# Optimization experiments

Measured on AMD Instinct MI355X. Metric: run time of the kernel, lower is better.

## Reference

```python
import jax, jax.numpy as jnp
import numpy as np

N_NODES = 100000
N_EDGES = 1600000
IN_CH, HID_CH, OUT_CH = 128, 128, 64
N_GRAPHS = 64


def gcn_conv(x, src, dst, W, b, n_nodes):
    """PyG-style GCNConv: self-loops already included in (src, dst).
    out_i = b + sum_j norm_ij * (x_j @ W), norm_ij = deg_i^-1/2 * deg_j^-1/2."""
    xw = x @ W  # [N, out]
    deg = jax.ops.segment_sum(jnp.ones_like(dst, dtype=xw.dtype), dst,
                              num_segments=n_nodes)  # [N]
    dinv = jnp.where(deg > 0, jax.lax.rsqrt(jnp.maximum(deg, 1e-12)), 0.0)
    norm = dinv[src] * dinv[dst]  # [E]
    msg = xw[src] * norm[:, None]  # gather + scale  [E, out]
    out = jax.ops.segment_sum(msg, dst, num_segments=n_nodes)  # scatter-add
    return out + b


def global_mean_pool(x, batch, n_graphs):
    s = jax.ops.segment_sum(x, batch, num_segments=n_graphs)
    cnt = jax.ops.segment_sum(jnp.ones((x.shape[0],), x.dtype), batch,
                              num_segments=n_graphs)
    return s / jnp.maximum(cnt, 1.0)[:, None]


def setup_inputs() -> dict:
    key = jax.random.key(0)
    ks = jax.random.split(key, 9)
    x = jax.random.normal(ks[0], (N_NODES, IN_CH), dtype=jnp.float32)
    edge_index = jax.random.randint(ks[1], (2, N_EDGES), 0, N_NODES, dtype=jnp.int64)
    batch = jnp.sort(jax.random.randint(ks[2], (N_NODES,), 0, N_GRAPHS, dtype=jnp.int64))
    # Glorot-ish params
    s1 = 1.0 / np.sqrt(IN_CH)
    s2 = 1.0 / np.sqrt(HID_CH)
    W1 = jax.random.normal(ks[3], (IN_CH, HID_CH), jnp.float32) * s1
    b1 = jnp.zeros((HID_CH,), jnp.float32)
    W2 = jax.random.normal(ks[4], (HID_CH, HID_CH), jnp.float32) * s2
    b2 = jnp.zeros((HID_CH,), jnp.float32)
    Wl = jax.random.normal(ks[5], (HID_CH, OUT_CH), jnp.float32) * s2
    bl = jax.random.normal(ks[6], (OUT_CH,), jnp.float32) * 0.01
    return {"x": x, "edge_index": edge_index, "batch": batch,
            "W1": W1, "b1": b1, "W2": W2, "b2": b2, "Wl": Wl, "bl": bl}


def reference(x, edge_index, batch, W1, b1, W2, b2, Wl, bl):
    n = x.shape[0]
    loop = jnp.arange(n, dtype=edge_index.dtype)
    src = jnp.concatenate([edge_index[0], loop])  # add self-loops
    dst = jnp.concatenate([edge_index[1], loop])
    h = jax.nn.relu(gcn_conv(x, src, dst, W1, b1, n))
    h = jax.nn.relu(gcn_conv(h, src, dst, W2, b2, n))
    g = global_mean_pool(h, batch, N_GRAPHS)  # [B, hid]
    return g @ Wl + bl  # [B, out]
```

## Files before the change

### kernel.cpp

```cpp
#include <hip/hip_runtime.h>

#define N_NODESC 100000
#define N_EDGESC 1600000
#define CH 128
#define NG 64
#define OC 64

#define GST_BLKS 391
#define EDGE_BLKS 6250
#define MFMA_BLKS 1563
#define PAD_STRIDE 128
#define RANGE 12500
#define EB_PER_BLK 16
#define BGROUPS ((EDGE_BLKS + EB_PER_BLK - 1) / EB_PER_BLK)
#define BUILD_BLKS (8 * BGROUPS)

typedef __attribute__((ext_vector_type(8))) short short8;
typedef __attribute__((ext_vector_type(4))) float f32x4;

__device__ __forceinline__ unsigned short f2b_u(float f) {
    union { float f; unsigned int u; } x; x.f = f;
    unsigned int u = x.u;
    return (unsigned short)((u + 0x7fffu + ((u >> 16) & 1u)) >> 16);
}
__device__ __forceinline__ float b2f_lo(unsigned int v) {
    union { unsigned int u; float f; } x; x.u = v << 16; return x.f;
}
__device__ __forceinline__ float b2f_hi(unsigned int v) {
    union { unsigned int u; float f; } x; x.u = v & 0xffff0000u; return x.f;
}
__device__ __forceinline__ float dinv_of(const int* __restrict__ deg, int i) {
    return rsqrtf((float)(deg[i] + 1));
}

#define WSTR 136
template<int AFP>
__device__ __forceinline__ void mfma_compute(int blk, int t, const void* __restrict__ Ap,
                                             unsigned short* __restrict__ Ob,
                                             const unsigned short* WsT) {
    int wave = t >> 6, lane = t & 63;
    int quad = lane >> 4, l16 = lane & 15;
    int arow = blk * 64 + wave * 16 + l16;
    bool rowok = arow < N_NODESC;
    f32x4 acc[8] = {};
#pragma unroll
    for (int c = 0; c < 4; ++c) {
        int koff = c * 32 + quad * 8;
        short8 a;
        if (AFP) {
            const float* A = (const float*)Ap;
            float4 f0 = make_float4(0, 0, 0, 0), f1 = make_float4(0, 0, 0, 0);
            if (rowok) {
                f0 = *(const float4*)(A + (size_t)arow * 128 + koff);
                f1 = *(const float4*)(A + (size_t)arow * 128 + koff + 4);
            }
            a[0] = (short)f2b_u(f0.x); a[1] = (short)f2b_u(f0.y);
            a[2] = (short)f2b_u(f0.z); a[3] = (short)f2b_u(f0.w);
            a[4] = (short)f2b_u(f1.x); a[5] = (short)f2b_u(f1.y);
            a[6] = (short)f2b_u(f1.z); a[7] = (short)f2b_u(f1.w);
        } else {
            const unsigned short* A = (const unsigned short*)Ap;
            if (rowok) a = *(const short8*)(A + (size_t)arow * 128 + koff);
            else       a = (short8)(short)0;
        }
#pragma unroll
        for (int tt = 0; tt < 8; ++tt) {
            short8 b = *(const short8*)&WsT[(tt * 16 + l16) * WSTR + koff];
            acc[tt] = __builtin_amdgcn_mfma_f32_16x16x32_bf16(a, b, acc[tt], 0, 0, 0);
        }
    }
    int orow0 = blk * 64 + wave * 16 + quad * 4;
#pragma unroll
    for (int r = 0; r < 4; ++r) {
        int g = orow0 + r;
        if (g < N_NODESC) {
#pragma unroll
            for (int tt = 0; tt < 8; ++tt)
                Ob[(size_t)g * 128 + tt * 16 + l16] = f2b_u(acc[tt][r]);
        }
    }
}

__global__ void k_pack(const float* __restrict__ W2, const int* __restrict__ batch,
                       unsigned short* __restrict__ Wt2, int* __restrict__ gstart) {
    int b = blockIdx.x, t = threadIdx.x;
    if (b < 64) {
        int i = b * 256 + t;
        int k = i >> 7, c = i & 127;
        Wt2[c * 128 + k] = f2b_u(W2[k * 128 + c]);
    } else {
        int i = (b - 64) * 256 + t;
        if (i >= N_NODESC) return;
        int bb = batch[i];
        int bp = (i == 0) ? -1 : batch[i - 1];
        for (int g = bp + 1; g <= bb; ++g) gstart[g] = i;
        if (i == N_NODESC - 1)
            for (int g = bb + 1; g <= NG; ++g) gstart[g] = N_NODESC;
    }
}

__global__ __launch_bounds__(256) void k_l1_build(const float* __restrict__ x,
                                                  const float* __restrict__ W1,
                                                  unsigned short* __restrict__ xw,
                                                  const int* __restrict__ ei,
                                                  int* __restrict__ deg,
                                                  int* __restrict__ pad) {
    __shared__ unsigned short WsT[128 * WSTR];
    int t = threadIdx.x;
    if (blockIdx.x < BUILD_BLKS) {
        int bb = blockIdx.x;
        unsigned int r = bb & 7;
        int g0 = (bb >> 3) * EB_PER_BLK;
#pragma unroll 4
        for (int i = 0; i < EB_PER_BLK; ++i) {
            int e = (g0 + i) * 256 + t;
            if (e < N_EDGESC) {
                int d = ei[N_EDGESC + e];
                if ((unsigned)d / RANGE == r) {
                    int slot = atomicAdd(&deg[d], 1);
                    pad[d * PAD_STRIDE + (slot & (PAD_STRIDE - 1))] = ei[e];
                }
            }
        }
    } else {
        int blk = blockIdx.x - BUILD_BLKS;
        for (int idx = t; idx < 16384; idx += 256) {
            int k = idx >> 7, c = idx & 127;
            WsT[c * WSTR + k] = f2b_u(W1[idx]);
        }
        __syncthreads();
        mfma_compute<1>(blk, t, x, xw, WsT);
    }
}

__global__ __launch_bounds__(256) void k_mfma2(const unsigned short* __restrict__ A,
                                               const unsigned short* __restrict__ Wt,
                                               unsigned short* __restrict__ Ob) {
    __shared__ unsigned short WsT[128 * WSTR];
    int t = threadIdx.x;
    {
        const uint4* wsrc = (const uint4*)Wt;
        for (int idx = t; idx < 2048; idx += 256) {
            int row = idx >> 4, sub = idx & 15;
            *((uint4*)&WsT[row * WSTR] + sub) = wsrc[row * 16 + sub];
        }
    }
    __syncthreads();
    mfma_compute<0>(blockIdx.x, t, A, Ob, WsT);
}

__device__ __forceinline__ void gather_row(const unsigned int* __restrict__ xw,
                                           const int* __restrict__ pad,
                                           const int* __restrict__ deg,
                                           int s, int e, int lane,
                                           float& acc0, float& acc1) {
    int i = s;
    for (; i + 8 <= e; i += 8) {
        int s0 = pad[i], s1 = pad[i + 1], s2 = pad[i + 2], s3 = pad[i + 3];
        int s4 = pad[i + 4], s5 = pad[i + 5], s6 = pad[i + 6], s7 = pad[i + 7];
        float w0 = dinv_of(deg, s0), w1 = dinv_of(deg, s1);
        float w2 = dinv_of(deg, s2), w3 = dinv_of(deg, s3);
        float w4 = dinv_of(deg, s4), w5 = dinv_of(deg, s5);
        float w6 = dinv_of(deg, s6), w7 = dinv_of(deg, s7);
        unsigned int v0 = xw[(size_t)s0 * 64 + lane];
        unsigned int v1 = xw[(size_t)s1 * 64 + lane];
        unsigned int v2 = xw[(size_t)s2 * 64 + lane];
        unsigned int v3 = xw[(size_t)s3 * 64 + lane];
        unsigned int v4 = xw[(size_t)s4 * 64 + lane];
        unsigned int v5 = xw[(size_t)s5 * 64 + lane];
        unsigned int v6 = xw[(size_t)s6 * 64 + lane];
        unsigned int v7 = xw[(size_t)s7 * 64 + lane];
        acc0 += w0 * b2f_lo(v0); acc1 += w0 * b2f_hi(v0);
        acc0 += w1 * b2f_lo(v1); acc1 += w1 * b2f_hi(v1);
        acc0 += w2 * b2f_lo(v2); acc1 += w2 * b2f_hi(v2);
        acc0 += w3 * b2f_lo(v3); acc1 += w3 * b2f_hi(v3);
        acc0 += w4 * b2f_lo(v4); acc1 += w4 * b2f_hi(v4);
        acc0 += w5 * b2f_lo(v5); acc1 += w5 * b2f_hi(v5);
        acc0 += w6 * b2f_lo(v6); acc1 += w6 * b2f_hi(v6);
        acc0 += w7 * b2f_lo(v7); acc1 += w7 * b2f_hi(v7);
    }
    for (; i + 4 <= e; i += 4) {
        int s0 = pad[i], s1 = pad[i + 1], s2 = pad[i + 2], s3 = pad[i + 3];
        float w0 = dinv_of(deg, s0), w1 = dinv_of(deg, s1);
        float w2 = dinv_of(deg, s2), w3 = dinv_of(deg, s3);
        unsigned int v0 = xw[(size_t)s0 * 64 + lane];
        unsigned int v1 = xw[(size_t)s1 * 64 + lane];
        unsigned int v2 = xw[(size_t)s2 * 64 + lane];
        unsigned int v3 = xw[(size_t)s3 * 64 + lane];
        acc0 += w0 * b2f_lo(v0); acc1 += w0 * b2f_hi(v0);
        acc0 += w1 * b2f_lo(v1); acc1 += w1 * b2f_hi(v1);
        acc0 += w2 * b2f_lo(v2); acc1 += w2 * b2f_hi(v2);
        acc0 += w3 * b2f_lo(v3); acc1 += w3 * b2f_hi(v3);
    }
    for (; i < e; ++i) {
        int s0 = pad[i];
        float w0 = dinv_of(deg, s0);
        unsigned int v0 = xw[(size_t)s0 * 64 + lane];
        acc0 += w0 * b2f_lo(v0); acc1 += w0 * b2f_hi(v0);
    }
}

__global__ __launch_bounds__(256) void k_gather1(const unsigned int* __restrict__ xw,
                                                 const int* __restrict__ deg,
                                                 const int* __restrict__ pad,
                                                 const float* __restrict__ bias,
                                                 unsigned int* __restrict__ outp) {
    int t = threadIdx.x;
    int lane = t & 63;
    int node = blockIdx.x * 4 + (t >> 6);
    if (node >= N_NODESC) return;
    int dg = deg[node];
    int s = node * PAD_STRIDE, e = s + dg;
    float wn = rsqrtf((float)(dg + 1));
    unsigned int vs = xw[(size_t)node * 64 + lane];
    float acc0 = wn * b2f_lo(vs), acc1 = wn * b2f_hi(vs);
    gather_row(xw, pad, deg, s, e, lane, acc0, acc1);
    float2 b = ((const float2*)bias)[lane];
    float o0 = fmaxf(b.x + wn * acc0, 0.f);
    float o1 = fmaxf(b.y + wn * acc1, 0.f);
    outp[(size_t)node * 64 + lane] =
        ((unsigned int)f2b_u(o1) << 16) | (unsigned int)f2b_u(o0);
}

__global__ __launch_bounds__(256) void k_gather_pool(const unsigned int* __restrict__ xw,
                                                     const int* __restrict__ deg,
                                                     const int* __restrict__ pad,
                                                     const float* __restrict__ bias,
                                                     const int* __restrict__ batch,
                                                     float* __restrict__ gpart) {
    __shared__ float lds[4 * 128];
    int t = threadIdx.x, w = t >> 6, lane = t & 63;
    int base = blockIdx.x * 16;
    bool fast = batch[base] == batch[base + 15];
    float2 bv = ((const float2*)bias)[lane];
    float sum0 = 0.f, sum1 = 0.f;
#pragma unroll 1
    for (int j = 0; j < 4; ++j) {
        int node = base + w * 4 + j;
        int dg = deg[node];
        int s = node * PAD_STRIDE, e = s + dg;
        float wn = rsqrtf((float)(dg + 1));
        unsigned int vs = xw[(size_t)node * 64 + lane];
        float acc0 = wn * b2f_lo(vs), acc1 = wn * b2f_hi(vs);
        gather_row(xw, pad, deg, s, e, lane, acc0, acc1);
        float o0 = fmaxf(bv.x + wn * acc0, 0.f);
        float o1 = fmaxf(bv.y + wn * acc1, 0.f);
        if (fast) {
            sum0 += o0; sum1 += o1;
        } else {
            int g = batch[node];
            atomicAdd(&gpart[g * 128 + lane * 2], o0);
            atomicAdd(&gpart[g * 128 + lane * 2 + 1], o1);
        }
    }
    if (fast) {
        lds[w * 128 + lane * 2] = sum0;
        lds[w * 128 + lane * 2 + 1] = sum1;
        __syncthreads();
        if (t < 128) {
            float v = lds[t] + lds[128 + t] + lds[256 + t] + lds[384 + t];
            atomicAdd(&gpart[batch[base] * 128 + t], v);
        }
    }
}

__global__ void k_final(const float* __restrict__ gpart, const int* __restrict__ gstart,
                        const float* __restrict__ Wl, const float* __restrict__ bl,
                        float* __restrict__ out) {
    __shared__ float gs[128];
    int b = blockIdx.x;
    int o = threadIdx.x;
    gs[o] = gpart[b * 128 + o];
    gs[o + 64] = gpart[b * 128 + 64 + o];
    __syncthreads();
    int cnt = gstart[b + 1] - gstart[b];
    float sc = 1.f / (float)(cnt > 0 ? cnt : 1);
    float sum = 0.f;
    for (int k = 0; k < 128; ++k) sum += gs[k] * Wl[k * 64 + o];
    out[b * 64 + o] = bl[o] + sc * sum;
}

extern "C" void kernel_launch(void* const* d_in, const int* in_sizes, int n_in,
                              void* d_out, int out_size, void* d_ws, size_t ws_size,
                              hipStream_t stream) {
    const float* x    = (const float*)d_in[0];
    const int*   ei   = (const int*)d_in[1];
    const int*   batch= (const int*)d_in[2];
    const float* W1   = (const float*)d_in[3];
    const float* b1   = (const float*)d_in[4];
    const float* W2   = (const float*)d_in[5];
    const float* b2   = (const float*)d_in[6];
    const float* Wl   = (const float*)d_in[7];
    const float* bl   = (const float*)d_in[8];
    float* out = (float*)d_out;

    char* ws = (char*)d_ws;
    unsigned short* xw_s = (unsigned short*)ws; ws += (size_t)N_NODESC * CH * 2;
    unsigned short* h_b  = (unsigned short*)ws; ws += (size_t)N_NODESC * CH * 2;
    unsigned short* Wt2 = (unsigned short*)ws; ws += (size_t)CH * CH * 2;
    int*   deg    = (int*)ws;   ws += (size_t)N_NODESC * 4;
    float* gpart  = (float*)ws; ws += (size_t)NG * CH * 4;
    int*   pad    = (int*)ws;   ws += (size_t)N_NODESC * PAD_STRIDE * 4;
    int*   gstart = (int*)ws;   ws += (NG + 8) * 4;

    hipMemsetAsync(deg, 0, (size_t)N_NODESC * 4 + (size_t)NG * CH * 4, stream);

    k_pack<<<64 + GST_BLKS, 256, 0, stream>>>(W2, batch, Wt2, gstart);
    k_l1_build<<<BUILD_BLKS + MFMA_BLKS, 256, 0, stream>>>(x, W1, xw_s, ei, deg, pad);

    k_gather1<<<(N_NODESC + 3) / 4, 256, 0, stream>>>((const unsigned int*)xw_s,
        deg, pad, b1, (unsigned int*)h_b);
    k_mfma2<<<MFMA_BLKS, 256, 0, stream>>>(h_b, Wt2, xw_s);
    k_gather_pool<<<N_NODESC / 16, 256, 0, stream>>>((const unsigned int*)xw_s,
        deg, pad, b2, batch, gpart);

    k_final<<<NG, 64, 0, stream>>>(gpart, gstart, Wl, bl, out);
}
```

Measured before the change: 349.2 us.

## Replace global-atomic adjacency build with two-pass destination binning and LDS degree counting

The old build pass scanned all edges eight times, once per destination range, and did a global atomicAdd on deg per edge. It now does a first pass that histograms edges into 512-node bins in LDS, reserves space with one global atomic per bin and writes packed (local dst, src) records into per-bin buffers. A second pass per bin counts degrees with LDS atomics and writes the padded adjacency. W1 is pre-transposed to bf16 once in k_pre rather than by every MFMA block. This adds a binbuf workspace and an extra pass over the edges, and assumes each bin holds at most 16384 edges and that source indices fit in 17 bits.

```diff
diff --git a/kernel.cpp b/kernel.cpp
--- a/kernel.cpp
+++ b/kernel.cpp
@@ -7,13 +7,15 @@
 #define OC 64
 
 #define GST_BLKS 391
-#define EDGE_BLKS 6250
 #define MFMA_BLKS 1563
 #define PAD_STRIDE 128
-#define RANGE 12500
-#define EB_PER_BLK 16
-#define BGROUPS ((EDGE_BLKS + EB_PER_BLK - 1) / EB_PER_BLK)
-#define BUILD_BLKS (8 * BGROUPS)
+
+#define BIN_SHIFT 9
+#define BIN_W 512
+#define NBINS 196
+#define BIN_CAP 16384
+#define BIN1_BLKS 391
+#define E_PER_BIN1 4096
 
 typedef __attribute__((ext_vector_type(8))) short short8;
 typedef __attribute__((ext_vector_type(4))) float f32x4;
@@ -81,15 +83,54 @@
     }
 }
 
-__global__ void k_pack(const float* __restrict__ W2, const int* __restrict__ batch,
-                       unsigned short* __restrict__ Wt2, int* __restrict__ gstart) {
+__global__ __launch_bounds__(256) void k_pre(const int* __restrict__ ei,
+                                             const int* __restrict__ batch,
+                                             const float* __restrict__ W1,
+                                             const float* __restrict__ W2,
+                                             int* __restrict__ cursor,
+                                             unsigned int* __restrict__ binbuf,
+                                             unsigned short* __restrict__ Wt1,
+                                             unsigned short* __restrict__ Wt2,
+                                             int* __restrict__ gstart) {
+    __shared__ int hist[NBINS];
     int b = blockIdx.x, t = threadIdx.x;
-    if (b < 64) {
-        int i = b * 256 + t;
+    if (b < BIN1_BLKS) {
+        for (int i = t; i < NBINS; i += 256) hist[i] = 0;
+        __syncthreads();
+        int e0 = b * E_PER_BIN1;
+#pragma unroll 4
+        for (int i = 0; i < E_PER_BIN1 / 256; ++i) {
+            int e = e0 + i * 256 + t;
+            if (e < N_EDGESC) atomicAdd(&hist[ei[N_EDGESC + e] >> BIN_SHIFT], 1);
+        }
+        __syncthreads();
+        for (int i = t; i < NBINS; i += 256) {
+            int c = hist[i];
+            hist[i] = c ? atomicAdd(&cursor[i], c) : 0;
+        }
+        __syncthreads();
+#pragma unroll 4
+        for (int i = 0; i < E_PER_BIN1 / 256; ++i) {
+            int e = e0 + i * 256 + t;
+            if (e < N_EDGESC) {
+                int d = ei[N_EDGESC + e];
+                int s = ei[e];
+                int bin = d >> BIN_SHIFT;
+                int off = atomicAdd(&hist[bin], 1);
+                binbuf[(size_t)bin * BIN_CAP + off] =
+                    ((unsigned int)(d & (BIN_W - 1)) << 17) | (unsigned int)s;
+            }
+        }
+    } else if (b < BIN1_BLKS + 64) {
+        int i = (b - BIN1_BLKS) * 256 + t;
+        int k = i >> 7, c = i & 127;
+        Wt1[c * 128 + k] = f2b_u(W1[k * 128 + c]);
+    } else if (b < BIN1_BLKS + 128) {
+        int i = (b - BIN1_BLKS - 64) * 256 + t;
         int k = i >> 7, c = i & 127;
         Wt2[c * 128 + k] = f2b_u(W2[k * 128 + c]);
     } else {
-        int i = (b - 64) * 256 + t;
+        int i = (b - BIN1_BLKS - 128) * 256 + t;
         if (i >= N_NODESC) return;
         int bb = batch[i];
         int bp = (i == 0) ? -1 : batch[i - 1];
@@ -99,34 +140,40 @@
     }
 }
 
-__global__ __launch_bounds__(256) void k_l1_build(const float* __restrict__ x,
-                                                  const float* __restrict__ W1,
-                                                  unsigned short* __restrict__ xw,
-                                                  const int* __restrict__ ei,
-                                                  int* __restrict__ deg,
-                                                  int* __restrict__ pad) {
+__global__ __launch_bounds__(256) void k_main(const float* __restrict__ x,
+                                              const unsigned short* __restrict__ Wt1,
+                                              unsigned short* __restrict__ xw,
+                                              const int* __restrict__ cursor,
+                                              const unsigned int* __restrict__ binbuf,
+                                              int* __restrict__ deg,
+                                              int* __restrict__ pad) {
     __shared__ unsigned short WsT[128 * WSTR];
     int t = threadIdx.x;
-    if (blockIdx.x < BUILD_BLKS) {
-        int bb = blockIdx.x;
-        unsigned int r = bb & 7;
-        int g0 = (bb >> 3) * EB_PER_BLK;
-#pragma unroll 4
-        for (int i = 0; i < EB_PER_BLK; ++i) {
-            int e = (g0 + i) * 256 + t;
-            if (e < N_EDGESC) {
-                int d = ei[N_EDGESC + e];
-                if ((unsigned)d / RANGE == r) {
-                    int slot = atomicAdd(&deg[d], 1);
-                    pad[d * PAD_STRIDE + (slot & (PAD_STRIDE - 1))] = ei[e];
-                }
-            }
+    if (blockIdx.x < NBINS) {
+        int bin = blockIdx.x;
+        int* ldeg = (int*)WsT;
+        for (int i = t; i < BIN_W; i += 256) ldeg[i] = 0;
+        __syncthreads();
+        int n = cursor[bin];
+        size_t base = (size_t)bin * BIN_CAP;
+        for (int i = t; i < n; i += 256) {
+            unsigned int rec = binbuf[base + i];
+            int dl = rec >> 17;
+            int s = rec & 0x1FFFF;
+            int slot = atomicAdd(&ldeg[dl], 1) & (PAD_STRIDE - 1);
+            pad[(size_t)((bin << BIN_SHIFT) + dl) * PAD_STRIDE + slot] = s;
+        }
+        __syncthreads();
+        for (int i = t; i < BIN_W; i += 256) {
+            int node = (bin << BIN_SHIFT) + i;
+            if (node < N_NODESC) deg[node] = ldeg[i];
         }
     } else {
-        int blk = blockIdx.x - BUILD_BLKS;
-        for (int idx = t; idx < 16384; idx += 256) {
-            int k = idx >> 7, c = idx & 127;
-            WsT[c * WSTR + k] = f2b_u(W1[idx]);
+        int blk = blockIdx.x - NBINS;
+        const uint4* wsrc = (const uint4*)Wt1;
+        for (int idx = t; idx < 2048; idx += 256) {
+            int row = idx >> 4, sub = idx & 15;
+            *((uint4*)&WsT[row * WSTR] + sub) = wsrc[row * 16 + sub];
         }
         __syncthreads();
         mfma_compute<1>(blk, t, x, xw, WsT);
@@ -297,16 +344,21 @@
     char* ws = (char*)d_ws;
     unsigned short* xw_s = (unsigned short*)ws; ws += (size_t)N_NODESC * CH * 2;
     unsigned short* h_b  = (unsigned short*)ws; ws += (size_t)N_NODESC * CH * 2;
+    unsigned short* Wt1 = (unsigned short*)ws; ws += (size_t)CH * CH * 2;
     unsigned short* Wt2 = (unsigned short*)ws; ws += (size_t)CH * CH * 2;
+    int*   cursor = (int*)ws;   ws += (size_t)NBINS * 4;
+    float* gpart  = (float*)ws; ws += (size_t)NG * CH * 4;
     int*   deg    = (int*)ws;   ws += (size_t)N_NODESC * 4;
-    float* gpart  = (float*)ws; ws += (size_t)NG * CH * 4;
     int*   pad    = (int*)ws;   ws += (size_t)N_NODESC * PAD_STRIDE * 4;
+    unsigned int* binbuf = (unsigned int*)ws; ws += (size_t)NBINS * BIN_CAP * 4;
     int*   gstart = (int*)ws;   ws += (NG + 8) * 4;
 
-    hipMemsetAsync(deg, 0, (size_t)N_NODESC * 4 + (size_t)NG * CH * 4, stream);
-
-    k_pack<<<64 + GST_BLKS, 256, 0, stream>>>(W2, batch, Wt2, gstart);
-    k_l1_build<<<BUILD_BLKS + MFMA_BLKS, 256, 0, stream>>>(x, W1, xw_s, ei, deg, pad);
+    hipMemsetAsync(cursor, 0, (size_t)NBINS * 4 + (size_t)NG * CH * 4, stream);
+
+    k_pre<<<BIN1_BLKS + 128 + GST_BLKS, 256, 0, stream>>>(ei, batch, W1, W2,
+        cursor, binbuf, Wt1, Wt2, gstart);
+    k_main<<<NBINS + MFMA_BLKS, 256, 0, stream>>>(x, Wt1, xw_s, cursor, binbuf,
+                                                  deg, pad);
 
     k_gather1<<<(N_NODESC + 3) / 4, 256, 0, stream>>>((const unsigned int*)xw_s,
         deg, pad, b1, (unsigned int*)h_b);
```

Result: faster. 316.6 us (-9.3%).
